# Kernel optimization log

Hardware: AMD Instinct MI355X
Metric: run time of the kernel (lower is better)

The kernel has to match this reference:

```python
import jax, jax.numpy as jnp
import numpy as np
import math

D_MODEL = 1024
N_HEADS = 16
D_HEAD = 64


def setup_inputs() -> dict:
    key = jax.random.key(0)
    ks = jax.random.split(key, 9)
    B, T = 2, 2048
    s = 1.0 / math.sqrt(D_MODEL)
    return {
        "x": jax.random.normal(ks[0], (B, T, D_MODEL), dtype=jnp.float32),
        "Wq": jax.random.normal(ks[1], (D_MODEL, D_MODEL), dtype=jnp.float32) * s,
        "bq": jnp.zeros((D_MODEL,), dtype=jnp.float32),
        "Wk": jax.random.normal(ks[2], (D_MODEL, D_MODEL), dtype=jnp.float32) * s,
        "bk": jnp.zeros((D_MODEL,), dtype=jnp.float32),
        "Wv": jax.random.normal(ks[3], (D_MODEL, D_MODEL), dtype=jnp.float32) * s,
        "bv": jnp.zeros((D_MODEL,), dtype=jnp.float32),
        "Wo": jax.random.normal(ks[4], (D_MODEL, D_MODEL), dtype=jnp.float32) * s,
        "bo": jnp.zeros((D_MODEL,), dtype=jnp.float32),
    }


def reference(x, Wq, bq, Wk, bk, Wv, bv, Wo, bo):
    B, T, _ = x.shape
    # Linear layers (torch convention: y = x @ W^T + b)
    Q = x @ Wq.T + bq
    K = x @ Wk.T + bk
    V = x @ Wv.T + bv
    # [B, H, T, Dh]
    Q = Q.reshape(B, T, N_HEADS, D_HEAD).transpose(0, 2, 1, 3)
    K = K.reshape(B, T, N_HEADS, D_HEAD).transpose(0, 2, 1, 3)
    V = V.reshape(B, T, N_HEADS, D_HEAD).transpose(0, 2, 1, 3)
    scores = jnp.einsum("bhqd,bhkd->bhqk", Q, K) / math.sqrt(D_HEAD)
    causal_mask = jnp.tril(jnp.ones((T, T), dtype=bool))  # [T, T]
    scores = jnp.where(causal_mask, scores, -jnp.inf)
    attn = jax.nn.softmax(scores, axis=-1)
    out = jnp.einsum("bhqk,bhkd->bhqd", attn, V)
    out = out.transpose(0, 2, 1, 3).reshape(B, T, D_MODEL)
    return out @ Wo.T + bo
```

## Files before the change

kernel.cpp:

```cpp
#include <hip/hip_runtime.h>

typedef unsigned short u16;
typedef __bf16 bf16x8 __attribute__((ext_vector_type(8)));
typedef float f32x4 __attribute__((ext_vector_type(4)));
typedef float f32x16 __attribute__((ext_vector_type(16)));
typedef u16 u16x4 __attribute__((ext_vector_type(4)));
typedef unsigned int uint;

#define DM 1024
#define MROWS 4096
#define TSEQ 2048

static __device__ __forceinline__ u16 f2b(float f) {
  uint u = __builtin_bit_cast(uint, f);
  uint r = (u + 0x7fffu + ((u >> 16) & 1u)) >> 16;
  return (u16)r;
}

static __device__ __forceinline__ uint pkbf(float a, float b) {
  union { __bf16 h[2]; uint u; } x;
  x.h[0] = (__bf16)a; x.h[1] = (__bf16)b;
  return x.u;
}

__global__ __launch_bounds__(256) void cvt_all(
    const float* __restrict__ x, const float* __restrict__ w0,
    const float* __restrict__ w1, const float* __restrict__ w2,
    const float* __restrict__ w3, u16* __restrict__ xo, u16* __restrict__ o0,
    u16* __restrict__ o1, u16* __restrict__ o2, u16* __restrict__ o3,
    float s0) {
  const int bid = blockIdx.x;
  const float* in; u16* out; float scale = 1.0f; int i;
  if (bid < 4096) {
    in = x; out = xo; i = bid * 1024 + threadIdx.x * 4;
  } else {
    int sel = (bid - 4096) >> 10;
    in = (sel == 0) ? w0 : (sel == 1) ? w1 : (sel == 2) ? w2 : w3;
    out = (sel == 0) ? o0 : (sel == 1) ? o1 : (sel == 2) ? o2 : o3;
    if (sel == 0) scale = s0;
    i = ((bid - 4096) & 1023) * 1024 + threadIdx.x * 4;
  }
  float4 v = *(const float4*)(in + i);
  u16x4 o;
  o.x = f2b(v.x * scale); o.y = f2b(v.y * scale);
  o.z = f2b(v.z * scale); o.w = f2b(v.w * scale);
  *(u16x4*)(out + i) = o;
}

#define SWZ(o) ((o) ^ ((((o) >> 7) & 3) << 4))

static __device__ __forceinline__ void gemm_tile(const u16* __restrict__ A,
                                                 const u16* __restrict__ W,
                                                 int row0, int col0,
                                                 char* lds,
                                                 f32x4 (&acc)[4][4]) {
  const int tid = threadIdx.x;
  const int lane = tid & 63, wid = tid >> 6;
  const int wr = wid >> 1, wc = wid & 1;
  const int lg = lane >> 4, lr = lane & 15;

  const u16* srcA[2]; const u16* srcB[2]; int dst[2];
#pragma unroll
  for (int c = 0; c < 2; ++c) {
    int lin = (c * 256 + tid) * 16;
    int p = SWZ(lin);
    srcA[c] = A + (size_t)(row0 + (p >> 6)) * DM + ((p & 63) >> 1);
    srcB[c] = W + (size_t)(col0 + (p >> 6)) * DM + ((p & 63) >> 1);
    dst[c] = lin;
  }
  int offA[4], offB[4];
#pragma unroll
  for (int m = 0; m < 4; ++m) offA[m] = SWZ((wr * 64 + m * 16 + lr) * 64 + lg * 16);
#pragma unroll
  for (int n = 0; n < 4; ++n) offB[n] = SWZ((wc * 64 + n * 16 + lr) * 64 + lg * 16);

  f32x4 z = {0.f, 0.f, 0.f, 0.f};
#pragma unroll
  for (int m = 0; m < 4; ++m)
#pragma unroll
    for (int n = 0; n < 4; ++n) acc[m][n] = z;

  auto stage = [&](int k0, int buf) {
    char* bA = lds + buf * 16384;
    char* bB = bA + 8192;
#pragma unroll
    for (int c = 0; c < 2; ++c) {
      __builtin_amdgcn_global_load_lds(
          (const __attribute__((address_space(1))) void*)(srcA[c] + k0),
          (__attribute__((address_space(3))) void*)(bA + dst[c]), 16, 0, 0);
      __builtin_amdgcn_global_load_lds(
          (const __attribute__((address_space(1))) void*)(srcB[c] + k0),
          (__attribute__((address_space(3))) void*)(bB + dst[c]), 16, 0, 0);
    }
  };

  stage(0, 0);
  __syncthreads();
  int cur = 0;
  for (int k0 = 0; k0 < DM; k0 += 32) {
    if (k0 + 32 < DM) stage(k0 + 32, cur ^ 1);
    char* bA = lds + cur * 16384;
    char* bB = bA + 8192;
    bf16x8 av[4], bv[4];
#pragma unroll
    for (int m = 0; m < 4; ++m) av[m] = *(const bf16x8*)(bA + offA[m]);
#pragma unroll
    for (int n = 0; n < 4; ++n) bv[n] = *(const bf16x8*)(bB + offB[n]);
    __builtin_amdgcn_s_setprio(1);
#pragma unroll
    for (int m = 0; m < 4; ++m)
#pragma unroll
      for (int n = 0; n < 4; ++n)
        acc[m][n] = __builtin_amdgcn_mfma_f32_16x16x32_bf16(av[m], bv[n], acc[m][n], 0, 0, 0);
    __builtin_amdgcn_s_setprio(0);
    __syncthreads();
    cur ^= 1;
  }
}

__global__ __launch_bounds__(256) void qkv_gemm(
    const u16* __restrict__ xb, const u16* __restrict__ Wqb,
    const u16* __restrict__ Wkb, const u16* __restrict__ Wvb,
    const float* __restrict__ bq, const float* __restrict__ bk,
    const float* __restrict__ bv, u16* __restrict__ Qx, u16* __restrict__ Kx,
    u16* __restrict__ Vx) {
  __shared__ char lds[32768];
  const int seg = blockIdx.x >> 3, nt = blockIdx.x & 7;
  const int row0 = blockIdx.y * 128, col0 = nt * 128;
  const u16* W = (seg == 0) ? Wqb : (seg == 1) ? Wkb : Wvb;
  const float* bias = (seg == 0) ? bq : (seg == 1) ? bk : bv;
  const float bscale = (seg == 0) ? 0.18033688011112042f : 1.0f;

  f32x4 acc[4][4];
  gemm_tile(xb, W, row0, col0, lds, acc);

  const int tid = threadIdx.x;
  const int lane = tid & 63, wid = tid >> 6;
  const int wr = wid >> 1, wc = wid & 1;
  const int lg = lane >> 4, lr = lane & 15;

  float bcol[4];
#pragma unroll
  for (int n = 0; n < 4; ++n) bcol[n] = bias[col0 + wc * 64 + n * 16 + lr] * bscale;

  if (seg < 2) {
#pragma unroll
    for (int m = 0; m < 4; ++m)
#pragma unroll
      for (int n = 0; n < 4; ++n) {
        int colB = (wc * 64 + n * 16 + lr) * 2;
#pragma unroll
        for (int r = 0; r < 4; ++r) {
          int row = wr * 64 + m * 16 + lg * 4 + r;
          *(u16*)(lds + row * 256 + (colB ^ ((row & 7) << 4))) =
              f2b(acc[m][n][r] + bcol[n]);
        }
      }
  } else {
    const int hi2 = lg & 1, jh = lg >> 1;
#pragma unroll
    for (int m = 0; m < 4; ++m) {
      const int c = m & 1;
      const int ktl = wr * 2 + (m >> 1);
#pragma unroll
      for (int n = 0; n < 4; ++n) {
        int col = wc * 64 + n * 16 + lr;
        int hloc = col >> 6, dcol = col & 63;
        int hh = dcol >> 5, dp = dcol & 31;
        int byte = (hloc * 4 + ktl) * 4096 + (((c * 2 + hh) * 2 + hi2) * 512) +
                   dp * 16 + jh * 8;
        byte ^= ((dp & 3) << 5) ^ (hi2 << 6);
        u16x4 pk;
        pk.x = f2b(acc[m][n][0] + bcol[n]);
        pk.y = f2b(acc[m][n][1] + bcol[n]);
        pk.z = f2b(acc[m][n][2] + bcol[n]);
        pk.w = f2b(acc[m][n][3] + bcol[n]);
        *(u16x4*)(lds + byte) = pk;
      }
    }
  }
  __syncthreads();

  const int st = tid >> 5, lnq = tid & 31;
  const int bI = row0 >> 11;
  if (seg < 2) {
    u16* out = (seg == 0) ? Qx : Kx;
    const int hloc = st & 1, twloc = st >> 1;
    const int h = (col0 >> 6) + hloc;
    const int tw = ((row0 & 2047) >> 5) + twloc;
    u16* base = out + ((size_t)(bI * 16 + h) * 64 + tw) * 2048;
#pragma unroll
    for (int ch = 0; ch < 8; ++ch) {
      int q = ch * 256 + lnq * 8;
      int c = q >> 9, hi2 = (q >> 8) & 1;
      int row = twloc * 32 + lnq;
      int colB = hloc * 128 + c * 32 + hi2 * 16;
      bf16x8 v = *(const bf16x8*)(lds + row * 256 + (colB ^ ((row & 7) << 4)));
      *(bf16x8*)(base + q) = v;
    }
  } else {
    const int hloc = st & 1, ktl = st >> 1;
    const int h = (col0 >> 6) + hloc;
    const int kt = ((row0 & 2047) >> 5) + ktl;
    u16* base = Vx + ((size_t)(bI * 16 + h) * 64 + kt) * 2048;
#pragma unroll
    for (int ch = 0; ch < 8; ++ch) {
      int hi2 = ch & 1;
      int byte = (hloc * 4 + ktl) * 4096 + ch * 512 + lnq * 16;
      byte ^= ((lnq & 3) << 5) ^ (hi2 << 6);
      bf16x8 v = *(const bf16x8*)(lds + byte);
      *(bf16x8*)(base + ch * 256 + lnq * 8) = v;
    }
  }
}

__global__ __launch_bounds__(256, 4) void attn_kernel(const u16* __restrict__ Qx,
                                                      const u16* __restrict__ Kx,
                                                      const u16* __restrict__ Vx,
                                                      u16* __restrict__ Aout) {
  __shared__ float mrg[2][64][32];
  __shared__ float mml[2][64][2];
  const int tid = threadIdx.x, lane = tid & 63, wid = tid >> 6;
  const int hi = lane >> 5, ln = lane & 31;
  const int half = wid & 1, spl = wid >> 1;
  const int id = blockIdx.x + (blockIdx.y << 5);
  const int xcd = id & 7, idx = id >> 3;
  const int bh = xcd * 4 + (idx & 3);
  const int qt = 31 - (idx >> 2);
  const int b = bh >> 4, h = bh & 15;
  const int q0 = qt * 64 + half * 32;
  const int ntile = (q0 >> 5) + 1;
  const int halfn = (ntile + 1) >> 1;
  const int tbeg = spl ? halfn : 0;
  const int tend = spl ? ntile : halfn;

  const u16* Qp = Qx + ((size_t)bh * 64 + (q0 >> 5)) * 2048;
  const u16* Kt = Kx + (size_t)bh * 64 * 2048;
  const u16* Vt = Vx + (size_t)bh * 64 * 2048;

  bf16x8 qf[4];
#pragma unroll
  for (int c = 0; c < 4; ++c)
    qf[c] = *(const bf16x8*)(Qp + c * 512 + hi * 256 + ln * 8);

  f32x16 Oa, Ob;
#pragma unroll
  for (int r = 0; r < 16; ++r) { Oa[r] = 0.f; Ob[r] = 0.f; }
  float m = -1e30f, l = 0.f;

  bf16x8 kf[4], vf[4];
  auto loadK = [&](int kt) {
    const u16* Kp = Kt + (size_t)kt * 2048;
#pragma unroll
    for (int c = 0; c < 4; ++c)
      kf[c] = *(const bf16x8*)(Kp + c * 512 + hi * 256 + ln * 8);
  };
  auto loadV = [&](int kt) {
    const u16* Vp = Vt + (size_t)kt * 2048;
#pragma unroll
    for (int c = 0; c < 4; ++c)
      vf[c] = *(const bf16x8*)(Vp + c * 512 + hi * 256 + ln * 8);
  };

  if (tbeg < tend) loadK(tbeg);
  for (int kt = tbeg; kt < tend; ++kt) {
    loadV(kt);
    f32x16 S;
#pragma unroll
    for (int r = 0; r < 16; ++r) S[r] = 0.f;
    __builtin_amdgcn_s_setprio(1);
#pragma unroll
    for (int c = 0; c < 4; ++c)
      S = __builtin_amdgcn_mfma_f32_32x32x16_bf16(kf[c], qf[c], S, 0, 0, 0);
    __builtin_amdgcn_s_setprio(0);
    if (kt + 1 < tend) loadK(kt + 1);
    if (kt == ntile - 1) {
      const int q = q0 + ln;
#pragma unroll
      for (int r = 0; r < 16; ++r) {
        int kv = kt * 32 + (r & 3) + 8 * (r >> 2) + 4 * hi;
        if (kv > q) S[r] = -1e38f;
      }
    }
    float a0 = fmaxf(fmaxf(S[0], S[1]), S[2]);
    float a1 = fmaxf(fmaxf(S[3], S[4]), S[5]);
    float a2 = fmaxf(fmaxf(S[6], S[7]), S[8]);
    float a3 = fmaxf(fmaxf(S[9], S[10]), S[11]);
    float a4 = fmaxf(fmaxf(S[12], S[13]), S[14]);
    float mx = fmaxf(fmaxf(fmaxf(a0, a1), fmaxf(a2, a3)), fmaxf(a4, S[15]));
    if (!__all(mx - m <= 8.f)) {
      float nm = fmaxf(m, mx);
      nm = fmaxf(nm, __shfl_xor(nm, 32));
      float sf = __builtin_amdgcn_exp2f(m - nm);
      m = nm; l *= sf;
#pragma unroll
      for (int r = 0; r < 16; ++r) { Oa[r] *= sf; Ob[r] *= sf; }
    }
#pragma unroll
    for (int r = 0; r < 16; ++r) S[r] = __builtin_amdgcn_exp2f(S[r] - m);
    float ts = ((S[0] + S[1]) + (S[2] + S[3])) + ((S[4] + S[5]) + (S[6] + S[7]));
    ts += ((S[8] + S[9]) + (S[10] + S[11])) + ((S[12] + S[13]) + (S[14] + S[15]));
    l += ts;
    uint pw[8];
#pragma unroll
    for (int i = 0; i < 8; ++i) pw[i] = pkbf(S[2 * i], S[2 * i + 1]);
    __builtin_amdgcn_s_setprio(1);
#pragma unroll
    for (int c = 0; c < 2; ++c) {
      union { uint w[4]; bf16x8 v; } pf;
      pf.w[0] = pw[4 * c + 0]; pf.w[1] = pw[4 * c + 1];
      pf.w[2] = pw[4 * c + 2]; pf.w[3] = pw[4 * c + 3];
      Oa = __builtin_amdgcn_mfma_f32_32x32x16_bf16(vf[2 * c + 0], pf.v, Oa, 0, 0, 0);
      Ob = __builtin_amdgcn_mfma_f32_32x32x16_bf16(vf[2 * c + 1], pf.v, Ob, 0, 0, 0);
    }
    __builtin_amdgcn_s_setprio(0);
  }

  union uo { f32x16 v; f32x4 q[4]; };
  const int sw8 = lane & 7;
  char* moc = (char*)&mrg[half][0][0];
  if (spl == 1) {
    uo ua, ub; ua.v = Oa; ub.v = Ob;
#pragma unroll
    for (int c = 0; c < 4; ++c) {
      *(f32x4*)(moc + lane * 128 + ((c ^ sw8) * 16)) = ua.q[c];
      *(f32x4*)(moc + lane * 128 + (((c + 4) ^ sw8) * 16)) = ub.q[c];
    }
    mml[half][lane][0] = m;
    mml[half][lane][1] = l;
  }
  __syncthreads();
  if (spl == 1) return;

  {
    float mY = mml[half][lane][0], lY = mml[half][lane][1];
    f32x4 rb[8];
#pragma unroll
    for (int c = 0; c < 8; ++c)
      rb[c] = *(const f32x4*)(moc + lane * 128 + ((c ^ sw8) * 16));
    float M = fmaxf(m, mY);
    float eX = __builtin_amdgcn_exp2f(m - M);
    float eY = __builtin_amdgcn_exp2f(mY - M);
    uo ua, ub; ua.v = Oa; ub.v = Ob;
#pragma unroll
    for (int c = 0; c < 4; ++c) {
      ua.q[c] = ua.q[c] * eX + rb[c] * eY;
      ub.q[c] = ub.q[c] * eX + rb[c + 4] * eY;
    }
    Oa = ua.v; Ob = ub.v;
    l = l * eX + lY * eY;
  }

  float lr = l + __shfl_xor(l, 32);
  const float inv = 1.f / lr;

  __threadfence_block();
  char* Tc = moc;
#pragma unroll
  for (int i = 0; i < 8; ++i) {
    int d0 = (2 * i & 3) + 8 * ((2 * i) >> 2) + 4 * hi;
    uint wA = pkbf(Oa[2 * i] * inv, Oa[2 * i + 1] * inv);
    *(uint*)(Tc + (ln * 128 + ((d0 * 2) ^ ((ln & 7) << 4)))) = wA;
    uint wB = pkbf(Ob[2 * i] * inv, Ob[2 * i + 1] * inv);
    *(uint*)(Tc + (ln * 128 + (((d0 + 32) * 2) ^ ((ln & 7) << 4)))) = wB;
  }
  __threadfence_block();
  u16* Ap = Aout + (size_t)b * TSEQ * DM + h * 64 + (size_t)(q0 + ln) * DM;
#pragma unroll
  for (int j = 0; j < 4; ++j) {
    int oct = hi * 4 + j;
    bf16x8 v = *(const bf16x8*)(Tc + (ln * 128 + ((oct * 16) ^ ((ln & 7) << 4))));
    *(bf16x8*)(Ap + oct * 8) = v;
  }
}

__global__ __launch_bounds__(256) void out_gemm(const u16* __restrict__ attn,
                                                const u16* __restrict__ Wob,
                                                const float* __restrict__ bo,
                                                float* __restrict__ out) {
  __shared__ char lds[32768];
  const int row0 = blockIdx.y * 128, col0 = blockIdx.x * 128;
  f32x4 acc[4][4];
  gemm_tile(attn, Wob, row0, col0, lds, acc);

  const int tid = threadIdx.x;
  const int lane = tid & 63, wid = tid >> 6;
  const int wr = wid >> 1, wc = wid & 1;
  const int lg = lane >> 4, lr = lane & 15;
#pragma unroll
  for (int m = 0; m < 4; ++m)
#pragma unroll
    for (int n = 0; n < 4; ++n) {
      int col = col0 + wc * 64 + n * 16 + lr;
      float b = bo[col];
#pragma unroll
      for (int r = 0; r < 4; ++r) {
        int row = row0 + wr * 64 + m * 16 + lg * 4 + r;
        out[(size_t)row * DM + col] = acc[m][n][r] + b;
      }
    }
}

extern "C" void kernel_launch(void* const* d_in, const int* in_sizes, int n_in,
                              void* d_out, int out_size, void* d_ws, size_t ws_size,
                              hipStream_t stream) {
  const float* x = (const float*)d_in[0];
  const float* Wq = (const float*)d_in[1];
  const float* bq = (const float*)d_in[2];
  const float* Wk = (const float*)d_in[3];
  const float* bk = (const float*)d_in[4];
  const float* Wv = (const float*)d_in[5];
  const float* bv = (const float*)d_in[6];
  const float* Wo = (const float*)d_in[7];
  const float* bo = (const float*)d_in[8];

  char* ws = (char*)d_ws;
  const size_t MB = 1024 * 1024;
  u16* xb = (u16*)(ws);
  u16* Wqb = (u16*)(ws + 8 * MB);
  u16* Wkb = (u16*)(ws + 10 * MB);
  u16* Wvb = (u16*)(ws + 12 * MB);
  u16* Wob = (u16*)(ws + 14 * MB);
  u16* Qf = (u16*)(ws + 16 * MB);
  u16* Kf = (u16*)(ws + 24 * MB);
  u16* Vf = (u16*)(ws + 32 * MB);
  u16* attnb = xb;

  cvt_all<<<8192, 256, 0, stream>>>(x, Wq, Wk, Wv, Wo, xb, Wqb, Wkb, Wvb, Wob,
                                    0.18033688011112042f);

  qkv_gemm<<<dim3(24, 32), 256, 0, stream>>>(xb, Wqb, Wkb, Wvb, bq, bk, bv, Qf, Kf, Vf);
  attn_kernel<<<dim3(32, 32), 256, 0, stream>>>(Qf, Kf, Vf, attnb);
  out_gemm<<<dim3(8, 32), 256, 0, stream>>>(attnb, Wob, bo, (float*)d_out);
}
```

Measured before the change: 92.35 us.

## Split each 32-row query tile across four waves and pair short/long tiles per block

The attention kernel now gives each block two 32-row query tiles, one long (63-p) and one short (p), processed one after the other. For each tile the causal KV range is split four ways across the block's waves, and the partial softmax states are combined by a tree merge through shared memory. This aims to even out work across blocks and waves under the causal mask. In exchange it adds extra __syncthreads, LDS merge traffic, and a serial loop over the two tiles inside each block.

```diff
diff --git a/kernel.cpp b/kernel.cpp
--- a/kernel.cpp
+++ b/kernel.cpp
@@ -218,159 +218,172 @@
                                                       const u16* __restrict__ Kx,
                                                       const u16* __restrict__ Vx,
                                                       u16* __restrict__ Aout) {
-  __shared__ float mrg[2][64][32];
-  __shared__ float mml[2][64][2];
-  const int tid = threadIdx.x, lane = tid & 63, wid = tid >> 6;
+  __shared__ float bufA[64][32];
+  __shared__ float bufB[64][32];
+  __shared__ float mmlA[64][2], mmlB[64][2];
+  const int tid = threadIdx.x, lane = tid & 63, spl = tid >> 6;
   const int hi = lane >> 5, ln = lane & 31;
-  const int half = wid & 1, spl = wid >> 1;
   const int id = blockIdx.x + (blockIdx.y << 5);
   const int xcd = id & 7, idx = id >> 3;
   const int bh = xcd * 4 + (idx & 3);
-  const int qt = 31 - (idx >> 2);
+  const int p = idx >> 2;
   const int b = bh >> 4, h = bh & 15;
-  const int q0 = qt * 64 + half * 32;
-  const int ntile = (q0 >> 5) + 1;
-  const int halfn = (ntile + 1) >> 1;
-  const int tbeg = spl ? halfn : 0;
-  const int tend = spl ? ntile : halfn;
-
-  const u16* Qp = Qx + ((size_t)bh * 64 + (q0 >> 5)) * 2048;
+  const int sw8 = lane & 7;
+
   const u16* Kt = Kx + (size_t)bh * 64 * 2048;
   const u16* Vt = Vx + (size_t)bh * 64 * 2048;
 
-  bf16x8 qf[4];
-#pragma unroll
-  for (int c = 0; c < 4; ++c)
-    qf[c] = *(const bf16x8*)(Qp + c * 512 + hi * 256 + ln * 8);
-
-  f32x16 Oa, Ob;
-#pragma unroll
-  for (int r = 0; r < 16; ++r) { Oa[r] = 0.f; Ob[r] = 0.f; }
-  float m = -1e30f, l = 0.f;
-
-  bf16x8 kf[4], vf[4];
-  auto loadK = [&](int kt) {
-    const u16* Kp = Kt + (size_t)kt * 2048;
+  for (int it = 0; it < 2; ++it) {
+    const int qt32 = it ? p : 63 - p;
+    const int q0 = qt32 * 32;
+    const int ntile = qt32 + 1;
+    const int tbeg = (spl * ntile) >> 2;
+    const int tend = ((spl + 1) * ntile) >> 2;
+
+    const u16* Qp = Qx + ((size_t)bh * 64 + qt32) * 2048;
+    bf16x8 qf[4];
 #pragma unroll
     for (int c = 0; c < 4; ++c)
-      kf[c] = *(const bf16x8*)(Kp + c * 512 + hi * 256 + ln * 8);
-  };
-  auto loadV = [&](int kt) {
-    const u16* Vp = Vt + (size_t)kt * 2048;
-#pragma unroll
-    for (int c = 0; c < 4; ++c)
-      vf[c] = *(const bf16x8*)(Vp + c * 512 + hi * 256 + ln * 8);
-  };
-
-  if (tbeg < tend) loadK(tbeg);
-  for (int kt = tbeg; kt < tend; ++kt) {
-    loadV(kt);
-    f32x16 S;
-#pragma unroll
-    for (int r = 0; r < 16; ++r) S[r] = 0.f;
-    __builtin_amdgcn_s_setprio(1);
-#pragma unroll
-    for (int c = 0; c < 4; ++c)
-      S = __builtin_amdgcn_mfma_f32_32x32x16_bf16(kf[c], qf[c], S, 0, 0, 0);
-    __builtin_amdgcn_s_setprio(0);
-    if (kt + 1 < tend) loadK(kt + 1);
-    if (kt == ntile - 1) {
-      const int q = q0 + ln;
-#pragma unroll
-      for (int r = 0; r < 16; ++r) {
-        int kv = kt * 32 + (r & 3) + 8 * (r >> 2) + 4 * hi;
-        if (kv > q) S[r] = -1e38f;
-      }
-    }
-    float a0 = fmaxf(fmaxf(S[0], S[1]), S[2]);
-    float a1 = fmaxf(fmaxf(S[3], S[4]), S[5]);
-    float a2 = fmaxf(fmaxf(S[6], S[7]), S[8]);
-    float a3 = fmaxf(fmaxf(S[9], S[10]), S[11]);
-    float a4 = fmaxf(fmaxf(S[12], S[13]), S[14]);
-    float mx = fmaxf(fmaxf(fmaxf(a0, a1), fmaxf(a2, a3)), fmaxf(a4, S[15]));
-    if (!__all(mx - m <= 8.f)) {
-      float nm = fmaxf(m, mx);
-      nm = fmaxf(nm, __shfl_xor(nm, 32));
-      float sf = __builtin_amdgcn_exp2f(m - nm);
-      m = nm; l *= sf;
-#pragma unroll
-      for (int r = 0; r < 16; ++r) { Oa[r] *= sf; Ob[r] *= sf; }
-    }
-#pragma unroll
-    for (int r = 0; r < 16; ++r) S[r] = __builtin_amdgcn_exp2f(S[r] - m);
-    float ts = ((S[0] + S[1]) + (S[2] + S[3])) + ((S[4] + S[5]) + (S[6] + S[7]));
-    ts += ((S[8] + S[9]) + (S[10] + S[11])) + ((S[12] + S[13]) + (S[14] + S[15]));
-    l += ts;
-    uint pw[8];
-#pragma unroll
-    for (int i = 0; i < 8; ++i) pw[i] = pkbf(S[2 * i], S[2 * i + 1]);
-    __builtin_amdgcn_s_setprio(1);
-#pragma unroll
-    for (int c = 0; c < 2; ++c) {
-      union { uint w[4]; bf16x8 v; } pf;
-      pf.w[0] = pw[4 * c + 0]; pf.w[1] = pw[4 * c + 1];
-      pf.w[2] = pw[4 * c + 2]; pf.w[3] = pw[4 * c + 3];
-      Oa = __builtin_amdgcn_mfma_f32_32x32x16_bf16(vf[2 * c + 0], pf.v, Oa, 0, 0, 0);
-      Ob = __builtin_amdgcn_mfma_f32_32x32x16_bf16(vf[2 * c + 1], pf.v, Ob, 0, 0, 0);
-    }
-    __builtin_amdgcn_s_setprio(0);
-  }
-
-  union uo { f32x16 v; f32x4 q[4]; };
-  const int sw8 = lane & 7;
-  char* moc = (char*)&mrg[half][0][0];
-  if (spl == 1) {
-    uo ua, ub; ua.v = Oa; ub.v = Ob;
-#pragma unroll
-    for (int c = 0; c < 4; ++c) {
-      *(f32x4*)(moc + lane * 128 + ((c ^ sw8) * 16)) = ua.q[c];
-      *(f32x4*)(moc + lane * 128 + (((c + 4) ^ sw8) * 16)) = ub.q[c];
-    }
-    mml[half][lane][0] = m;
-    mml[half][lane][1] = l;
-  }
-  __syncthreads();
-  if (spl == 1) return;
-
-  {
-    float mY = mml[half][lane][0], lY = mml[half][lane][1];
-    f32x4 rb[8];
-#pragma unroll
-    for (int c = 0; c < 8; ++c)
-      rb[c] = *(const f32x4*)(moc + lane * 128 + ((c ^ sw8) * 16));
-    float M = fmaxf(m, mY);
-    float eX = __builtin_amdgcn_exp2f(m - M);
-    float eY = __builtin_amdgcn_exp2f(mY - M);
-    uo ua, ub; ua.v = Oa; ub.v = Ob;
-#pragma unroll
-    for (int c = 0; c < 4; ++c) {
-      ua.q[c] = ua.q[c] * eX + rb[c] * eY;
-      ub.q[c] = ub.q[c] * eX + rb[c + 4] * eY;
-    }
-    Oa = ua.v; Ob = ub.v;
-    l = l * eX + lY * eY;
-  }
-
-  float lr = l + __shfl_xor(l, 32);
-  const float inv = 1.f / lr;
-
-  __threadfence_block();
-  char* Tc = moc;
-#pragma unroll
-  for (int i = 0; i < 8; ++i) {
-    int d0 = (2 * i & 3) + 8 * ((2 * i) >> 2) + 4 * hi;
-    uint wA = pkbf(Oa[2 * i] * inv, Oa[2 * i + 1] * inv);
-    *(uint*)(Tc + (ln * 128 + ((d0 * 2) ^ ((ln & 7) << 4)))) = wA;
-    uint wB = pkbf(Ob[2 * i] * inv, Ob[2 * i + 1] * inv);
-    *(uint*)(Tc + (ln * 128 + (((d0 + 32) * 2) ^ ((ln & 7) << 4)))) = wB;
-  }
-  __threadfence_block();
-  u16* Ap = Aout + (size_t)b * TSEQ * DM + h * 64 + (size_t)(q0 + ln) * DM;
-#pragma unroll
-  for (int j = 0; j < 4; ++j) {
-    int oct = hi * 4 + j;
-    bf16x8 v = *(const bf16x8*)(Tc + (ln * 128 + ((oct * 16) ^ ((ln & 7) << 4))));
-    *(bf16x8*)(Ap + oct * 8) = v;
+      qf[c] = *(const bf16x8*)(Qp + c * 512 + hi * 256 + ln * 8);
+
+    f32x16 Oa, Ob;
+#pragma unroll
+    for (int r = 0; r < 16; ++r) { Oa[r] = 0.f; Ob[r] = 0.f; }
+    float m = -1e30f, l = 0.f;
+
+    bf16x8 kf[4], vf[4];
+    auto loadK = [&](int kt) {
+      const u16* Kp = Kt + (size_t)kt * 2048;
+#pragma unroll
+      for (int c = 0; c < 4; ++c)
+        kf[c] = *(const bf16x8*)(Kp + c * 512 + hi * 256 + ln * 8);
+    };
+    auto loadV = [&](int kt) {
+      const u16* Vp = Vt + (size_t)kt * 2048;
+#pragma unroll
+      for (int c = 0; c < 4; ++c)
+        vf[c] = *(const bf16x8*)(Vp + c * 512 + hi * 256 + ln * 8);
+    };
+
+    if (tbeg < tend) loadK(tbeg);
+    for (int kt = tbeg; kt < tend; ++kt) {
+      loadV(kt);
+      f32x16 S;
+#pragma unroll
+      for (int r = 0; r < 16; ++r) S[r] = 0.f;
+      __builtin_amdgcn_s_setprio(1);
+#pragma unroll
+      for (int c = 0; c < 4; ++c)
+        S = __builtin_amdgcn_mfma_f32_32x32x16_bf16(kf[c], qf[c], S, 0, 0, 0);
+      __builtin_amdgcn_s_setprio(0);
+      if (kt + 1 < tend) loadK(kt + 1);
+      if (kt == ntile - 1) {
+        const int q = q0 + ln;
+#pragma unroll
+        for (int r = 0; r < 16; ++r) {
+          int kv = kt * 32 + (r & 3) + 8 * (r >> 2) + 4 * hi;
+          if (kv > q) S[r] = -1e38f;
+        }
+      }
+      float a0 = fmaxf(fmaxf(S[0], S[1]), S[2]);
+      float a1 = fmaxf(fmaxf(S[3], S[4]), S[5]);
+      float a2 = fmaxf(fmaxf(S[6], S[7]), S[8]);
+      float a3 = fmaxf(fmaxf(S[9], S[10]), S[11]);
+      float a4 = fmaxf(fmaxf(S[12], S[13]), S[14]);
+      float mx = fmaxf(fmaxf(fmaxf(a0, a1), fmaxf(a2, a3)), fmaxf(a4, S[15]));
+      if (!__all(mx - m <= 8.f)) {
+        float nm = fmaxf(m, mx);
+        nm = fmaxf(nm, __shfl_xor(nm, 32));
+        float sf = __builtin_amdgcn_exp2f(m - nm);
+        m = nm; l *= sf;
+#pragma unroll
+        for (int r = 0; r < 16; ++r) { Oa[r] *= sf; Ob[r] *= sf; }
+      }
+#pragma unroll
+      for (int r = 0; r < 16; ++r) S[r] = __builtin_amdgcn_exp2f(S[r] - m);
+      float ts = ((S[0] + S[1]) + (S[2] + S[3])) + ((S[4] + S[5]) + (S[6] + S[7]));
+      ts += ((S[8] + S[9]) + (S[10] + S[11])) + ((S[12] + S[13]) + (S[14] + S[15]));
+      l += ts;
+      uint pw[8];
+#pragma unroll
+      for (int i = 0; i < 8; ++i) pw[i] = pkbf(S[2 * i], S[2 * i + 1]);
+      __builtin_amdgcn_s_setprio(1);
+#pragma unroll
+      for (int c = 0; c < 2; ++c) {
+        union { uint w[4]; bf16x8 v; } pf;
+        pf.w[0] = pw[4 * c + 0]; pf.w[1] = pw[4 * c + 1];
+        pf.w[2] = pw[4 * c + 2]; pf.w[3] = pw[4 * c + 3];
+        Oa = __builtin_amdgcn_mfma_f32_32x32x16_bf16(vf[2 * c + 0], pf.v, Oa, 0, 0, 0);
+        Ob = __builtin_amdgcn_mfma_f32_32x32x16_bf16(vf[2 * c + 1], pf.v, Ob, 0, 0, 0);
+      }
+      __builtin_amdgcn_s_setprio(0);
+    }
+
+    union uo { f32x16 v; f32x4 q[4]; };
+    auto writePart = [&](float* buf, float* mml) {
+      uo ua, ub; ua.v = Oa; ub.v = Ob;
+      char* bc = (char*)buf;
+#pragma unroll
+      for (int c = 0; c < 4; ++c) {
+        *(f32x4*)(bc + lane * 128 + ((c ^ sw8) * 16)) = ua.q[c];
+        *(f32x4*)(bc + lane * 128 + (((c + 4) ^ sw8) * 16)) = ub.q[c];
+      }
+      mml[lane * 2 + 0] = m;
+      mml[lane * 2 + 1] = l;
+    };
+    auto mergePart = [&](const float* buf, const float* mml) {
+      float mY = mml[lane * 2 + 0], lY = mml[lane * 2 + 1];
+      const char* bc = (const char*)buf;
+      f32x4 rb[8];
+#pragma unroll
+      for (int c = 0; c < 8; ++c)
+        rb[c] = *(const f32x4*)(bc + lane * 128 + ((c ^ sw8) * 16));
+      float M = fmaxf(m, mY);
+      float eX = __builtin_amdgcn_exp2f(m - M);
+      float eY = __builtin_amdgcn_exp2f(mY - M);
+      uo ua, ub; ua.v = Oa; ub.v = Ob;
+#pragma unroll
+      for (int c = 0; c < 4; ++c) {
+        ua.q[c] = ua.q[c] * eX + rb[c] * eY;
+        ub.q[c] = ub.q[c] * eX + rb[c + 4] * eY;
+      }
+      Oa = ua.v; Ob = ub.v;
+      l = l * eX + lY * eY;
+      m = M;
+    };
+
+    if (spl == 1) writePart(&bufA[0][0], &mmlA[0][0]);
+    if (spl == 3) writePart(&bufB[0][0], &mmlB[0][0]);
+    __syncthreads();
+    if (spl == 0) mergePart(&bufA[0][0], &mmlA[0][0]);
+    if (spl == 2) mergePart(&bufB[0][0], &mmlB[0][0]);
+    __syncthreads();
+    if (spl == 2) writePart(&bufA[0][0], &mmlA[0][0]);
+    __syncthreads();
+    if (spl == 0) {
+      mergePart(&bufA[0][0], &mmlA[0][0]);
+      float lr = l + __shfl_xor(l, 32);
+      const float inv = 1.f / lr;
+      __threadfence_block();
+      char* Tc = (char*)&bufA[0][0];
+#pragma unroll
+      for (int i = 0; i < 8; ++i) {
+        int d0 = (2 * i & 3) + 8 * ((2 * i) >> 2) + 4 * hi;
+        uint wA = pkbf(Oa[2 * i] * inv, Oa[2 * i + 1] * inv);
+        *(uint*)(Tc + (ln * 128 + ((d0 * 2) ^ ((ln & 7) << 4)))) = wA;
+        uint wB = pkbf(Ob[2 * i] * inv, Ob[2 * i + 1] * inv);
+        *(uint*)(Tc + (ln * 128 + (((d0 + 32) * 2) ^ ((ln & 7) << 4)))) = wB;
+      }
+      __threadfence_block();
+      u16* Ap = Aout + (size_t)b * TSEQ * DM + h * 64 + (size_t)(q0 + ln) * DM;
+#pragma unroll
+      for (int j = 0; j < 4; ++j) {
+        int oct = hi * 4 + j;
+        bf16x8 v = *(const bf16x8*)(Tc + (ln * 128 + ((oct * 16) ^ ((ln & 7) << 4))));
+        *(bf16x8*)(Ap + oct * 8) = v;
+      }
+    }
+    __syncthreads();
   }
 }
 
```

Result: slower. 107.1 us (+16.0%).
